# Kernel optimization log

Hardware: AMD Instinct MI355X
Metric: run time of the kernel (lower is better)

Reference implementation:

```python
import jax, jax.numpy as jnp
import numpy as np

B, T, C = 2, 2048, 1024
N_HEADS = 16
HEAD_DIM = C // N_HEADS

def setup_inputs() -> dict:
    key = jax.random.key(0)
    k1, k2, k3 = jax.random.split(key, 3)
    x = jax.random.normal(k1, (B, T, C), dtype=jnp.float32)
    W_qkv = jax.random.normal(k2, (C, 3 * C), dtype=jnp.float32) * (1.0 / np.sqrt(C))
    W_out = jax.random.normal(k3, (C, C), dtype=jnp.float32) * (1.0 / np.sqrt(C))
    return {"x": x, "W_qkv": W_qkv, "W_out": W_out}

def reference(x, W_qkv, W_out):
    b, t, c = x.shape
    qkv = jnp.einsum('btc,cd->btd', x, W_qkv)  # [B,T,3C]
    q, k, v = jnp.split(qkv, 3, axis=-1)
    # [B, H, T, hd]
    q = q.reshape(b, t, N_HEADS, HEAD_DIM).transpose(0, 2, 1, 3)
    k = k.reshape(b, t, N_HEADS, HEAD_DIM).transpose(0, 2, 1, 3)
    v = v.reshape(b, t, N_HEADS, HEAD_DIM).transpose(0, 2, 1, 3)
    scale = 1.0 / jnp.sqrt(jnp.asarray(HEAD_DIM, dtype=x.dtype))
    attn = jnp.einsum('bhqd,bhkd->bhqk', q, k) * scale  # [B,H,T,T]
    causal = jnp.tril(jnp.ones((t, t), dtype=bool))
    attn = jnp.where(causal, attn, jnp.asarray(-1e9, dtype=attn.dtype))
    attn = jax.nn.softmax(attn, axis=-1)
    out = jnp.einsum('bhqk,bhkd->bhqd', attn, v)
    out = out.transpose(0, 2, 1, 3).reshape(b, t, c)
    return jnp.einsum('btc,cd->btd', out, W_out)
```

## Files before the change

### kernel.cpp

```cpp
#include <hip/hip_runtime.h>
#include <hip/hip_bf16.h>

typedef __attribute__((ext_vector_type(8))) short short8;
typedef __attribute__((ext_vector_type(4))) short bf16x4;
typedef __attribute__((ext_vector_type(4))) float floatx4;

#define T_SEQ 2048
#define NH    16
#define HD    64
#define QSCALE 0.18033688f

#define MFMA16(a, b, c) __builtin_amdgcn_mfma_f32_16x16x16bf16_1k(a, b, c, 0, 0, 0)

__device__ __forceinline__ ushort f2bf(float f) {
    union { float f; unsigned u; } un; un.f = f;
    unsigned r = un.u + 0x7fff + ((un.u >> 16) & 1);
    return (ushort)(r >> 16);
}
__device__ __forceinline__ unsigned pkbf(float a, float b) {
    __hip_bfloat162 t = __float22bfloat162_rn(float2{a, b});
    return *reinterpret_cast<unsigned*>(&t);
}

typedef const __attribute__((address_space(1))) unsigned int* gp1_t;
typedef __attribute__((address_space(3))) unsigned int* lp3_t;
__device__ __forceinline__ void gl_lds16(const ushort* g, ushort* l) {
    __builtin_amdgcn_global_load_lds((gp1_t)g, (lp3_t)l, 16, 0, 0);
}

__global__ void prep_kernel(const float* __restrict__ Wqkv, const float* __restrict__ Wout,
                            const float* __restrict__ x, ushort* __restrict__ wt_qkv,
                            ushort* __restrict__ wt_out, ushort* __restrict__ x_bf) {
    __shared__ ushort tile[32][33];
    const int bid = blockIdx.x;
    if (bid >= 4096) {
        size_t i = ((size_t)(bid - 4096) * 256 + threadIdx.x) * 8;
        float4 f0 = *(const float4*)(x + i);
        float4 f1 = *(const float4*)(x + i + 4);
        short8 v;
        v[0] = (short)f2bf(f0.x); v[1] = (short)f2bf(f0.y);
        v[2] = (short)f2bf(f0.z); v[3] = (short)f2bf(f0.w);
        v[4] = (short)f2bf(f1.x); v[5] = (short)f2bf(f1.y);
        v[6] = (short)f2bf(f1.z); v[7] = (short)f2bf(f1.w);
        *(short8*)(x_bf + i) = v;
        return;
    }
    const float* in; ushort* out; int R, C, gx, gy;
    if (bid < 3072) { in = Wqkv; out = wt_qkv; R = 1024; C = 3072; gx = bid % 96; gy = bid / 96; }
    else            { int t = bid - 3072; in = Wout; out = wt_out; R = 1024; C = 1024; gx = t & 31; gy = t >> 5; }
    const int tx = threadIdx.x & 31, ty = threadIdx.x >> 5;
    const int bx = gx * 32, by = gy * 32;
    #pragma unroll
    for (int i = ty; i < 32; i += 8)
        tile[i][tx] = f2bf(in[(size_t)(by + i) * C + bx + tx]);
    __syncthreads();
    #pragma unroll
    for (int i = ty; i < 32; i += 8)
        out[(size_t)(bx + i) * R + by + tx] = tile[tx][i];
}

template <int EPI>
__global__ __launch_bounds__(256, 2)
void gemm_bt(const ushort* __restrict__ A, const ushort* __restrict__ Bt,
             void* __restrict__ O0, ushort* __restrict__ O1, ushort* __restrict__ O2,
             int M, int N, int K) {
    __shared__ __align__(16) ushort smem[8704];
    ushort* As = smem;
    ushort* Bs = smem + 4096;
    const int tid  = threadIdx.x;
    const int wave = tid >> 6, lane = tid & 63;
    const int quad = lane >> 4, l16 = lane & 15;
    const int wm = (wave >> 1) * 64, wn = (wave & 1) * 64;
    const int m0 = blockIdx.x * 128, n0 = blockIdx.y * 128;

    const int c0 = tid, c1 = tid + 256;
    const int row0 = c0 >> 2, row1 = c1 >> 2;
    const int g0 = (((c0 & 3) ^ ((row0 >> 1) & 3))) * 8;
    const int g1 = (((c1 & 3) ^ ((row1 >> 1) & 3))) * 8;
    const ushort* aP0 = A  + (size_t)(m0 + row0) * K + g0;
    const ushort* aP1 = A  + (size_t)(m0 + row1) * K + g1;
    const ushort* bP0 = Bt + (size_t)(n0 + row0) * K + g0;
    const ushort* bP1 = Bt + (size_t)(n0 + row1) * K + g1;

    floatx4 acc[4][4];
    #pragma unroll
    for (int i = 0; i < 4; i++)
        #pragma unroll
        for (int j = 0; j < 4; j++)
            acc[i][j] = (floatx4){0.f, 0.f, 0.f, 0.f};

    const int col_sw = (quad ^ ((l16 >> 1) & 3)) * 8;

    for (int k0 = 0; k0 < K; k0 += 32) {
        __syncthreads();
        gl_lds16(aP0 + k0, &As[c0 * 8]);
        gl_lds16(aP1 + k0, &As[c1 * 8]);
        gl_lds16(bP0 + k0, &Bs[c0 * 8]);
        gl_lds16(bP1 + k0, &Bs[c1 * 8]);
        __syncthreads();
        short8 af[4], bf[4];
        #pragma unroll
        for (int i = 0; i < 4; i++)
            af[i] = *(const short8*)(&As[(wm + i * 16 + l16) * 32 + col_sw]);
        #pragma unroll
        for (int j = 0; j < 4; j++)
            bf[j] = *(const short8*)(&Bs[(wn + j * 16 + l16) * 32 + col_sw]);
        #pragma unroll
        for (int i = 0; i < 4; i++)
            #pragma unroll
            for (int j = 0; j < 4; j++)
                acc[i][j] = __builtin_amdgcn_mfma_f32_16x16x32_bf16(af[i], bf[j], acc[i][j], 0, 0, 0);
    }

    if (EPI == 0 && n0 >= 2048) {
        const int b = m0 >> 11;
        const int t0 = m0 & 2047;
        const int head0 = (n0 - 2048) >> 6;
        __syncthreads();
        #pragma unroll
        for (int nh = 0; nh < 2; nh++) {
            if ((wave & 1) == nh) {
                #pragma unroll
                for (int j = 0; j < 4; j++)
                    #pragma unroll
                    for (int i = 0; i < 4; i++) {
                        int nl = j * 16 + l16;
                        int mB = wm + i * 16 + quad * 4;
                        *(unsigned*)(&smem[nl * 136 + mB])     = pkbf(acc[i][j][0], acc[i][j][1]);
                        *(unsigned*)(&smem[nl * 136 + mB + 2]) = pkbf(acc[i][j][2], acc[i][j][3]);
                    }
            }
            __syncthreads();
            #pragma unroll
            for (int cc = 0; cc < 4; cc++) {
                int c = cc * 256 + tid;
                int row = c >> 4, mcol = (c & 15) * 8;
                uint4 v = *(const uint4*)(&smem[row * 136 + mcol]);
                *(uint4*)(&O2[((size_t)(b * NH + head0 + nh) * HD + row) * T_SEQ + t0 + mcol]) = v;
            }
            __syncthreads();
        }
        return;
    }

    #pragma unroll
    for (int i = 0; i < 4; i++) {
        #pragma unroll
        for (int j = 0; j < 4; j++) {
            #pragma unroll
            for (int r = 0; r < 4; r++) {
                int m = m0 + wm + i * 16 + quad * 4 + r;
                int n = n0 + wn + j * 16 + l16;
                if (EPI == 0) {
                    int b = m >> 11, t = m & 2047;
                    int part = n >> 10, c = n & 1023;
                    int head = c >> 6, off = c & 63;
                    float av = acc[i][j][r];
                    if (part == 0) av *= QSCALE;
                    ushort v = f2bf(av);
                    if (part == 0) ((ushort*)O0)[(((size_t)(b * NH + head)) * T_SEQ + t) * HD + off] = v;
                    else           O1[(((size_t)(b * NH + head)) * T_SEQ + t) * HD + off] = v;
                } else {
                    ((float*)O0)[(size_t)m * N + n] = acc[i][j][r];
                }
            }
        }
    }
}

__device__ __forceinline__ void softmax_step(floatx4 s[4], float& mst, float& lst,
                                             floatx4 o[4], bf16x4 pf[4]) {
    float t0 = fmaxf(fmaxf(s[0][0], s[0][1]), fmaxf(s[0][2], s[0][3]));
    float t1 = fmaxf(fmaxf(s[1][0], s[1][1]), fmaxf(s[1][2], s[1][3]));
    float t2 = fmaxf(fmaxf(s[2][0], s[2][1]), fmaxf(s[2][2], s[2][3]));
    float t3 = fmaxf(fmaxf(s[3][0], s[3][1]), fmaxf(s[3][2], s[3][3]));
    float t = fmaxf(fmaxf(t0, t1), fmaxf(t2, t3));
    t = fmaxf(t, __shfl_xor(t, 16));
    t = fmaxf(t, __shfl_xor(t, 32));
    float mnew  = fmaxf(mst, t);
    float alpha = exp2f(mst - mnew);
    mst = mnew;
    float lsum = 0.f;
    #pragma unroll
    for (int j = 0; j < 4; j++) {
        float p0 = exp2f(s[j][0] - mnew);
        float p1 = exp2f(s[j][1] - mnew);
        float p2 = exp2f(s[j][2] - mnew);
        float p3 = exp2f(s[j][3] - mnew);
        lsum += (p0 + p1) + (p2 + p3);
        union { bf16x4 v; unsigned u[2]; } pu;
        pu.u[0] = pkbf(p0, p1);
        pu.u[1] = pkbf(p2, p3);
        pf[j] = pu.v;
    }
    lsum += __shfl_xor(lsum, 16);
    lsum += __shfl_xor(lsum, 32);
    lst = lst * alpha + lsum;
    #pragma unroll
    for (int db = 0; db < 4; db++)
        #pragma unroll
        for (int r = 0; r < 4; r++) o[db][r] *= alpha;
}

__global__ __launch_bounds__(256, 4)
void attn_kernel(const ushort* __restrict__ Q, const ushort* __restrict__ Kk,
                 const ushort* __restrict__ Vt, ushort* __restrict__ Oout) {
    __shared__ __align__(16) ushort Ks[2][64 * 64];
    __shared__ __align__(16) ushort Vs[2][64 * 64];
    const int tid  = threadIdx.x;
    const int wave = tid >> 6, lane = tid & 63;
    const int quad = lane >> 4, l16 = lane & 15;
    const int idx = blockIdx.x;
    const int bh = idx & 31;
    const int j = idx >> 5;
    const int oct = j >> 3, r = j & 7;
    const int qt = (oct == 0) ? r : (oct == 1) ? (15 - r) : (oct == 2) ? (16 + r) : (31 - r);
    const int b = bh >> 4, h = bh & 15;

    const ushort* qp = Q  + (size_t)bh * T_SEQ * HD;
    const ushort* kp = Kk + (size_t)bh * T_SEQ * HD;
    const ushort* vp = Vt + (size_t)bh * HD * T_SEQ;

    const int q0w = qt * 64 + wave * 16;

    short8 qf[2];
    #pragma unroll
    for (int kb = 0; kb < 2; kb++)
        qf[kb] = *(const short8*)(qp + (size_t)(q0w + l16) * HD + kb * 32 + quad * 8);

    floatx4 o[4];
    #pragma unroll
    for (int db = 0; db < 4; db++) o[db] = (floatx4){0.f, 0.f, 0.f, 0.f};
    float mst = -1e30f, lst = 0.f;

    const int c0 = tid, c1 = tid + 256;
    const int r0 = c0 >> 3, r1 = c1 >> 3;
    const int g0 = ((c0 & 7) ^ (r0 & 7)) * 8;
    const int g1 = ((c1 & 7) ^ (r1 & 7)) * 8;
    const size_t koff0 = (size_t)r0 * HD + g0,     koff1 = (size_t)r1 * HD + g1;
    const size_t voff0 = (size_t)r0 * T_SEQ + g0,  voff1 = (size_t)r1 * T_SEQ + g1;

    gl_lds16(kp + koff0, &Ks[0][c0 * 8]);
    gl_lds16(kp + koff1, &Ks[0][c1 * 8]);
    gl_lds16(vp + voff0, &Vs[0][c0 * 8]);
    gl_lds16(vp + voff1, &Vs[0][c1 * 8]);

    const int xsw = (l16 & 7), qh = quad >> 1, ql = quad & 1;
    const int ka0 = l16 * 64 + ((quad ^ xsw) * 8);
    const int ka1 = l16 * 64 + (((4 + quad) ^ xsw) * 8);
    int va[4];
    #pragma unroll
    for (int jj = 0; jj < 4; jj++)
        va[jj] = l16 * 64 + (((2 * jj + qh) ^ xsw) * 8) + ql * 4;

#define ATT_STEP(BUF, KT)                                                        \
    {                                                                            \
        __syncthreads();                                                         \
        if ((KT) < qt) {                                                         \
            const size_t kbase = (size_t)((KT) + 1) * 64 * HD;                   \
            const int    vbase = ((KT) + 1) * 64;                                \
            gl_lds16(kp + kbase + koff0, &Ks[(BUF) ^ 1][c0 * 8]);                \
            gl_lds16(kp + kbase + koff1, &Ks[(BUF) ^ 1][c1 * 8]);                \
            gl_lds16(vp + vbase + voff0, &Vs[(BUF) ^ 1][c0 * 8]);                \
            gl_lds16(vp + vbase + voff1, &Vs[(BUF) ^ 1][c1 * 8]);                \
        }                                                                        \
        floatx4 s[4];                                                            \
        _Pragma("unroll")                                                        \
        for (int jj = 0; jj < 4; jj++) s[jj] = (floatx4){0.f, 0.f, 0.f, 0.f};    \
        _Pragma("unroll")                                                        \
        for (int jj = 0; jj < 4; jj++) {                                         \
            short8 kf0 = *(const short8*)(&Ks[BUF][ka0 + jj * 1024]);            \
            s[jj] = __builtin_amdgcn_mfma_f32_16x16x32_bf16(kf0, qf[0], s[jj], 0, 0, 0); \
        }                                                                        \
        _Pragma("unroll")                                                        \
        for (int jj = 0; jj < 4; jj++) {                                         \
            short8 kf1 = *(const short8*)(&Ks[BUF][ka1 + jj * 1024]);            \
            s[jj] = __builtin_amdgcn_mfma_f32_16x16x32_bf16(kf1, qf[1], s[jj], 0, 0, 0); \
        }                                                                        \
        if ((KT) == qt) {                                                        \
            _Pragma("unroll")                                                    \
            for (int jj = 0; jj < 4; jj++)                                       \
                _Pragma("unroll")                                                \
                for (int rr = 0; rr < 4; rr++) {                                 \
                    int key = (KT) * 64 + jj * 16 + quad * 4 + rr;               \
                    if (key > q0w + l16) s[jj][rr] = -1e30f;                     \
                }                                                                \
        }                                                                        \
        bf16x4 pf[4];                                                            \
        softmax_step(s, mst, lst, o, pf);                                        \
        _Pragma("unroll")                                                        \
        for (int jj = 0; jj < 4; jj++)                                           \
            _Pragma("unroll")                                                    \
            for (int db = 0; db < 4; db++) {                                     \
                bf16x4 vf = *(const bf16x4*)(&Vs[BUF][va[jj] + db * 1024]);      \
                o[db] = MFMA16(vf, pf[jj], o[db]);                               \
            }                                                                    \
    }

    int kt = 0;
    for (; kt + 1 <= qt; kt += 2) {
        ATT_STEP(0, kt)
        ATT_STEP(1, kt + 1)
    }
    if (kt <= qt) ATT_STEP(0, kt)
#undef ATT_STEP

    const float inv = 1.0f / lst;
    const int t = q0w + l16;
    #pragma unroll
    for (int db = 0; db < 4; db++) {
        union { ushort4 w; unsigned u[2]; } ou;
        ou.u[0] = pkbf(o[db][0] * inv, o[db][1] * inv);
        ou.u[1] = pkbf(o[db][2] * inv, o[db][3] * inv);
        *(ushort4*)(Oout + (((size_t)b * T_SEQ + t) * NH + h) * HD + db * 16 + quad * 4) = ou.w;
    }
}

extern "C" void kernel_launch(void* const* d_in, const int* in_sizes, int n_in,
                              void* d_out, int out_size, void* d_ws, size_t ws_size,
                              hipStream_t stream) {
    const float* x    = (const float*)d_in[0];
    const float* Wqkv = (const float*)d_in[1];
    const float* Wout = (const float*)d_in[2];
    ushort* ws = (ushort*)d_ws;

    ushort* wt_qkv = ws;
    ushort* wt_out = wt_qkv + 3072 * 1024;
    ushort* q_ws   = wt_out + 1024 * 1024;
    ushort* k_ws   = q_ws + 4194304;
    ushort* v_t    = k_ws + 4194304;
    ushort* a_out  = v_t + 4194304;
    ushort* x_bf   = a_out + 4194304;

    prep_kernel<<<dim3(6144), 256, 0, stream>>>(Wqkv, Wout, x, wt_qkv, wt_out, x_bf);

    gemm_bt<0><<<dim3(32, 24), 256, 0, stream>>>(x_bf, wt_qkv, q_ws, k_ws, v_t, 4096, 3072, 1024);

    attn_kernel<<<dim3(1024), 256, 0, stream>>>(q_ws, k_ws, v_t, a_out);

    gemm_bt<1><<<dim3(32, 8), 256, 0, stream>>>(a_out, wt_out, (float*)d_out, nullptr, nullptr,
                                                4096, 1024, 1024);
}
```

Measured before the change: 187.8 us.

## Split long causal query tiles across two blocks, merge partials, and tune softmax rescaling

Query tiles 16-31 are each split into two key-range halves processed by separate blocks. Each half writes unnormalized partial outputs plus running max and sum to workspace, and a new merge kernel combines them. Short tiles run unsplit in longest-first order, and the grid grows from 1024 to 1536 blocks, aiming to even out per-block work and tail latency. The change also skips the accumulator rescale when no lane's running max increases, switches to the raw hardware exp2 builtin, and raises launch-bound occupancy hints on both the GEMM and attention kernels. In exchange it adds an extra kernel launch and a round-trip of fp32 partials through global memory.

```diff
diff --git a/kernel.cpp b/kernel.cpp
--- a/kernel.cpp
+++ b/kernel.cpp
@@ -9,6 +9,7 @@
 #define NH    16
 #define HD    64
 #define QSCALE 0.18033688f
+#define EXP2(x) __builtin_amdgcn_exp2f(x)
 
 #define MFMA16(a, b, c) __builtin_amdgcn_mfma_f32_16x16x16bf16_1k(a, b, c, 0, 0, 0)
 
@@ -60,7 +61,7 @@
 }
 
 template <int EPI>
-__global__ __launch_bounds__(256, 2)
+__global__ __launch_bounds__(256, 3)
 void gemm_bt(const ushort* __restrict__ A, const ushort* __restrict__ Bt,
              void* __restrict__ O0, ushort* __restrict__ O1, ushort* __restrict__ O2,
              int M, int N, int K) {
@@ -177,16 +178,15 @@
     float t = fmaxf(fmaxf(t0, t1), fmaxf(t2, t3));
     t = fmaxf(t, __shfl_xor(t, 16));
     t = fmaxf(t, __shfl_xor(t, 32));
-    float mnew  = fmaxf(mst, t);
-    float alpha = exp2f(mst - mnew);
-    mst = mnew;
+    const bool nm = t > mst;
+    const float mnew = nm ? t : mst;
     float lsum = 0.f;
     #pragma unroll
     for (int j = 0; j < 4; j++) {
-        float p0 = exp2f(s[j][0] - mnew);
-        float p1 = exp2f(s[j][1] - mnew);
-        float p2 = exp2f(s[j][2] - mnew);
-        float p3 = exp2f(s[j][3] - mnew);
+        float p0 = EXP2(s[j][0] - mnew);
+        float p1 = EXP2(s[j][1] - mnew);
+        float p2 = EXP2(s[j][2] - mnew);
+        float p3 = EXP2(s[j][3] - mnew);
         lsum += (p0 + p1) + (p2 + p3);
         union { bf16x4 v; unsigned u[2]; } pu;
         pu.u[0] = pkbf(p0, p1);
@@ -195,27 +195,45 @@
     }
     lsum += __shfl_xor(lsum, 16);
     lsum += __shfl_xor(lsum, 32);
-    lst = lst * alpha + lsum;
-    #pragma unroll
-    for (int db = 0; db < 4; db++)
-        #pragma unroll
-        for (int r = 0; r < 4; r++) o[db][r] *= alpha;
-}
-
-__global__ __launch_bounds__(256, 4)
+    if (__ballot(nm)) {
+        float alpha = EXP2(mst - mnew);
+        mst = mnew;
+        lst = lst * alpha + lsum;
+        #pragma unroll
+        for (int db = 0; db < 4; db++)
+            #pragma unroll
+            for (int r = 0; r < 4; r++) o[db][r] *= alpha;
+    } else {
+        lst += lsum;
+    }
+}
+
+__global__ __launch_bounds__(256, 5)
 void attn_kernel(const ushort* __restrict__ Q, const ushort* __restrict__ Kk,
-                 const ushort* __restrict__ Vt, ushort* __restrict__ Oout) {
-    __shared__ __align__(16) ushort Ks[2][64 * 64];
-    __shared__ __align__(16) ushort Vs[2][64 * 64];
+                 const ushort* __restrict__ Vt, ushort* __restrict__ Oout,
+                 float* __restrict__ pm, float* __restrict__ pl, float* __restrict__ po) {
+    __shared__ __align__(16) ushort KsA[8192];
+    __shared__ __align__(16) ushort VsA[8192];
     const int tid  = threadIdx.x;
     const int wave = tid >> 6, lane = tid & 63;
     const int quad = lane >> 4, l16 = lane & 15;
     const int idx = blockIdx.x;
-    const int bh = idx & 31;
-    const int j = idx >> 5;
-    const int oct = j >> 3, r = j & 7;
-    const int qt = (oct == 0) ? r : (oct == 1) ? (15 - r) : (oct == 2) ? (16 + r) : (31 - r);
+    const int c = idx >> 5, bh = idx & 31;
     const int b = bh >> 4, h = bh & 15;
+
+    int qt, kb, ke, slot = 0;
+    bool partial;
+    if (c < 32) {
+        const int half = c & 1;
+        qt = 31 - (c >> 1);
+        const int hi = (qt + 2) >> 1;
+        if (half == 0) { kb = 0;  ke = hi - 1; }
+        else           { kb = hi; ke = qt;     }
+        partial = true;
+        slot = (bh * 16 + (qt - 16)) * 2 + half;
+    } else {
+        qt = 47 - c; kb = 0; ke = qt; partial = false;
+    }
 
     const ushort* qp = Q  + (size_t)bh * T_SEQ * HD;
     const ushort* kp = Kk + (size_t)bh * T_SEQ * HD;
@@ -225,8 +243,8 @@
 
     short8 qf[2];
     #pragma unroll
-    for (int kb = 0; kb < 2; kb++)
-        qf[kb] = *(const short8*)(qp + (size_t)(q0w + l16) * HD + kb * 32 + quad * 8);
+    for (int kbd = 0; kbd < 2; kbd++)
+        qf[kbd] = *(const short8*)(qp + (size_t)(q0w + l16) * HD + kbd * 32 + quad * 8);
 
     floatx4 o[4];
     #pragma unroll
@@ -240,10 +258,14 @@
     const size_t koff0 = (size_t)r0 * HD + g0,     koff1 = (size_t)r1 * HD + g1;
     const size_t voff0 = (size_t)r0 * T_SEQ + g0,  voff1 = (size_t)r1 * T_SEQ + g1;
 
-    gl_lds16(kp + koff0, &Ks[0][c0 * 8]);
-    gl_lds16(kp + koff1, &Ks[0][c1 * 8]);
-    gl_lds16(vp + voff0, &Vs[0][c0 * 8]);
-    gl_lds16(vp + voff1, &Vs[0][c1 * 8]);
+    {
+        const size_t kst = (size_t)kb * 64 * HD;
+        const int    vst = kb * 64;
+        gl_lds16(kp + kst + koff0, &KsA[c0 * 8]);
+        gl_lds16(kp + kst + koff1, &KsA[c1 * 8]);
+        gl_lds16(vp + vst + voff0, &VsA[c0 * 8]);
+        gl_lds16(vp + vst + voff1, &VsA[c1 * 8]);
+    }
 
     const int xsw = (l16 & 7), qh = quad >> 1, ql = quad & 1;
     const int ka0 = l16 * 64 + ((quad ^ xsw) * 8);
@@ -253,66 +275,108 @@
     for (int jj = 0; jj < 4; jj++)
         va[jj] = l16 * 64 + (((2 * jj + qh) ^ xsw) * 8) + ql * 4;
 
-#define ATT_STEP(BUF, KT)                                                        \
-    {                                                                            \
-        __syncthreads();                                                         \
-        if ((KT) < qt) {                                                         \
-            const size_t kbase = (size_t)((KT) + 1) * 64 * HD;                   \
-            const int    vbase = ((KT) + 1) * 64;                                \
-            gl_lds16(kp + kbase + koff0, &Ks[(BUF) ^ 1][c0 * 8]);                \
-            gl_lds16(kp + kbase + koff1, &Ks[(BUF) ^ 1][c1 * 8]);                \
-            gl_lds16(vp + vbase + voff0, &Vs[(BUF) ^ 1][c0 * 8]);                \
-            gl_lds16(vp + vbase + voff1, &Vs[(BUF) ^ 1][c1 * 8]);                \
-        }                                                                        \
-        floatx4 s[4];                                                            \
-        _Pragma("unroll")                                                        \
-        for (int jj = 0; jj < 4; jj++) s[jj] = (floatx4){0.f, 0.f, 0.f, 0.f};    \
-        _Pragma("unroll")                                                        \
-        for (int jj = 0; jj < 4; jj++) {                                         \
-            short8 kf0 = *(const short8*)(&Ks[BUF][ka0 + jj * 1024]);            \
-            s[jj] = __builtin_amdgcn_mfma_f32_16x16x32_bf16(kf0, qf[0], s[jj], 0, 0, 0); \
-        }                                                                        \
-        _Pragma("unroll")                                                        \
-        for (int jj = 0; jj < 4; jj++) {                                         \
-            short8 kf1 = *(const short8*)(&Ks[BUF][ka1 + jj * 1024]);            \
-            s[jj] = __builtin_amdgcn_mfma_f32_16x16x32_bf16(kf1, qf[1], s[jj], 0, 0, 0); \
-        }                                                                        \
-        if ((KT) == qt) {                                                        \
-            _Pragma("unroll")                                                    \
-            for (int jj = 0; jj < 4; jj++)                                       \
-                _Pragma("unroll")                                                \
-                for (int rr = 0; rr < 4; rr++) {                                 \
-                    int key = (KT) * 64 + jj * 16 + quad * 4 + rr;               \
-                    if (key > q0w + l16) s[jj][rr] = -1e30f;                     \
-                }                                                                \
-        }                                                                        \
-        bf16x4 pf[4];                                                            \
-        softmax_step(s, mst, lst, o, pf);                                        \
-        _Pragma("unroll")                                                        \
-        for (int jj = 0; jj < 4; jj++)                                           \
-            _Pragma("unroll")                                                    \
-            for (int db = 0; db < 4; db++) {                                     \
-                bf16x4 vf = *(const bf16x4*)(&Vs[BUF][va[jj] + db * 1024]);      \
-                o[db] = MFMA16(vf, pf[jj], o[db]);                               \
-            }                                                                    \
-    }
-
-    int kt = 0;
-    for (; kt + 1 <= qt; kt += 2) {
-        ATT_STEP(0, kt)
-        ATT_STEP(1, kt + 1)
-    }
-    if (kt <= qt) ATT_STEP(0, kt)
-#undef ATT_STEP
-
-    const float inv = 1.0f / lst;
-    const int t = q0w + l16;
-    #pragma unroll
-    for (int db = 0; db < 4; db++) {
+    for (int kt = kb; kt <= ke; ++kt) {
+        const int bo = ((kt - kb) & 1) << 12;
+        __syncthreads();
+        if (kt < ke) {
+            const size_t kn = (size_t)(kt + 1) * 64 * HD;
+            const int    vn = (kt + 1) * 64;
+            const int    bn = bo ^ 4096;
+            gl_lds16(kp + kn + koff0, &KsA[bn + c0 * 8]);
+            gl_lds16(kp + kn + koff1, &KsA[bn + c1 * 8]);
+            gl_lds16(vp + vn + voff0, &VsA[bn + c0 * 8]);
+            gl_lds16(vp + vn + voff1, &VsA[bn + c1 * 8]);
+        }
+
+        floatx4 s[4];
+        #pragma unroll
+        for (int jj = 0; jj < 4; jj++) s[jj] = (floatx4){0.f, 0.f, 0.f, 0.f};
+        #pragma unroll
+        for (int jj = 0; jj < 4; jj++) {
+            short8 kf0 = *(const short8*)(&KsA[bo + ka0 + jj * 1024]);
+            s[jj] = __builtin_amdgcn_mfma_f32_16x16x32_bf16(kf0, qf[0], s[jj], 0, 0, 0);
+        }
+        #pragma unroll
+        for (int jj = 0; jj < 4; jj++) {
+            short8 kf1 = *(const short8*)(&KsA[bo + ka1 + jj * 1024]);
+            s[jj] = __builtin_amdgcn_mfma_f32_16x16x32_bf16(kf1, qf[1], s[jj], 0, 0, 0);
+        }
+
+        if (kt == qt) {
+            #pragma unroll
+            for (int jj = 0; jj < 4; jj++)
+                #pragma unroll
+                for (int rr = 0; rr < 4; rr++) {
+                    int key = kt * 64 + jj * 16 + quad * 4 + rr;
+                    if (key > q0w + l16) s[jj][rr] = -1e30f;
+                }
+        }
+
+        bf16x4 pf[4];
+        softmax_step(s, mst, lst, o, pf);
+
+        #pragma unroll
+        for (int jj = 0; jj < 4; jj++)
+            #pragma unroll
+            for (int db = 0; db < 4; db++) {
+                bf16x4 vf = *(const bf16x4*)(&VsA[bo + va[jj] + db * 1024]);
+                o[db] = MFMA16(vf, pf[jj], o[db]);
+            }
+    }
+
+    if (partial) {
+        const int row = wave * 16 + l16;
+        if (quad == 0) {
+            pm[slot * 64 + row] = mst;
+            pl[slot * 64 + row] = lst;
+        }
+        float* pob = po + (size_t)slot * 4096 + row * 64;
+        #pragma unroll
+        for (int db = 0; db < 4; db++)
+            *(float4*)(pob + db * 16 + quad * 4) =
+                (float4){o[db][0], o[db][1], o[db][2], o[db][3]};
+    } else {
+        const float inv = 1.0f / lst;
+        const int t = q0w + l16;
+        #pragma unroll
+        for (int db = 0; db < 4; db++) {
+            union { ushort4 w; unsigned u[2]; } ou;
+            ou.u[0] = pkbf(o[db][0] * inv, o[db][1] * inv);
+            ou.u[1] = pkbf(o[db][2] * inv, o[db][3] * inv);
+            *(ushort4*)(Oout + (((size_t)b * T_SEQ + t) * NH + h) * HD + db * 16 + quad * 4) = ou.w;
+        }
+    }
+}
+
+__global__ void attn_merge(const float* __restrict__ pm, const float* __restrict__ pl,
+                           const float* __restrict__ po, ushort* __restrict__ Oout) {
+    const int bid = blockIdx.x;
+    const int bh = bid >> 4, qidx = bid & 15;
+    const int qt = 16 + qidx;
+    const int b = bh >> 4, h = bh & 15;
+    const int tid = threadIdx.x;
+    const int row = tid >> 2, dq = (tid & 3) * 16;
+    const int s0 = (bh * 16 + qidx) * 2, s1 = s0 + 1;
+
+    const float m0 = pm[s0 * 64 + row], m1 = pm[s1 * 64 + row];
+    const float l0 = pl[s0 * 64 + row], l1 = pl[s1 * 64 + row];
+    const float m  = fmaxf(m0, m1);
+    const float a0 = EXP2(m0 - m), a1 = EXP2(m1 - m);
+    const float inv = 1.0f / (a0 * l0 + a1 * l1);
+    const float c0 = a0 * inv, c1 = a1 * inv;
+
+    const float* p0 = po + (size_t)s0 * 4096 + row * 64 + dq;
+    const float* p1 = po + (size_t)s1 * 4096 + row * 64 + dq;
+    const int t = qt * 64 + row;
+    ushort* op = Oout + (((size_t)b * T_SEQ + t) * NH + h) * HD + dq;
+    #pragma unroll
+    for (int i = 0; i < 4; i++) {
+        float4 f0 = *(const float4*)(p0 + i * 4);
+        float4 f1 = *(const float4*)(p1 + i * 4);
         union { ushort4 w; unsigned u[2]; } ou;
-        ou.u[0] = pkbf(o[db][0] * inv, o[db][1] * inv);
-        ou.u[1] = pkbf(o[db][2] * inv, o[db][3] * inv);
-        *(ushort4*)(Oout + (((size_t)b * T_SEQ + t) * NH + h) * HD + db * 16 + quad * 4) = ou.w;
+        ou.u[0] = pkbf(c0 * f0.x + c1 * f1.x, c0 * f0.y + c1 * f1.y);
+        ou.u[1] = pkbf(c0 * f0.z + c1 * f1.z, c0 * f0.w + c1 * f1.w);
+        *(ushort4*)(op + i * 4) = ou.w;
     }
 }
 
@@ -331,12 +395,16 @@
     ushort* v_t    = k_ws + 4194304;
     ushort* a_out  = v_t + 4194304;
     ushort* x_bf   = a_out + 4194304;
+    float*  pm     = (float*)(x_bf + 4194304);
+    float*  pl     = pm + 65536;
+    float*  po     = pl + 65536;
 
     prep_kernel<<<dim3(6144), 256, 0, stream>>>(Wqkv, Wout, x, wt_qkv, wt_out, x_bf);
 
     gemm_bt<0><<<dim3(32, 24), 256, 0, stream>>>(x_bf, wt_qkv, q_ws, k_ws, v_t, 4096, 3072, 1024);
 
-    attn_kernel<<<dim3(1024), 256, 0, stream>>>(q_ws, k_ws, v_t, a_out);
+    attn_kernel<<<dim3(1536), 256, 0, stream>>>(q_ws, k_ws, v_t, a_out, pm, pl, po);
+    attn_merge<<<dim3(512), 256, 0, stream>>>(pm, pl, po, a_out);
 
     gemm_bt<1><<<dim3(32, 8), 256, 0, stream>>>(a_out, wt_out, (float*)d_out, nullptr, nullptr,
                                                 4096, 1024, 1024);
```

Result: no change. 189.2 us (+0.8%).
